# Kernel optimization log

Hardware: AMD Instinct MI355X
Metric: run time of the kernel (lower is better)

## Reference

```python
import jax, jax.numpy as jnp
import numpy as np

N, C, H, W, J = 16, 8, 512, 1024, 8


def setup_inputs() -> dict:
    key = jax.random.key(0)
    logits = jax.random.normal(key, (N, C, H, W), dtype=jnp.float32)
    rng = np.random.default_rng(0)
    start = rng.integers(0, H - 2, size=(N, J))
    length = rng.integers(1, H // 2, size=(N, J))
    end = np.minimum(start + length, H - 1)          # ensure z+1 <= H-1
    ch = rng.integers(0, C, size=(N, J))
    params = jnp.asarray(np.stack([start, end, ch], axis=-1).astype(np.int32))
    return {"logits": logits, "params": params}


def reference(logits, params):
    n, c, h, w = logits.shape
    probs = jax.nn.softmax(logits, axis=-1)
    # soft-argmax expected position over grid axis -> [n, c, h]
    pos = jnp.sum(probs * jnp.arange(w, dtype=logits.dtype), axis=-1)
    # adjacent-row position differences -> [n, c, h-1]
    diff = pos[:, :, :-1] - pos[:, :, 1:]
    start = params[..., 0]   # [n, J]
    end = params[..., 1]     # [n, J]
    ch = params[..., 2]      # [n, J]
    # gather the channel for each (sample, lane): [n, J, h-1]
    diff_g = jnp.take_along_axis(diff, ch[:, :, None].astype(jnp.int32), axis=1)
    z = jnp.arange(h - 1, dtype=jnp.int32)
    mask = (z[None, None, :] >= start[:, :, None]) & (z[None, None, :] < end[:, :, None])
    # smooth_l1 vs zeros, mean over the ragged selected elements
    x = jnp.abs(diff_g)
    sl1 = jnp.where(x < 1.0, 0.5 * diff_g * diff_g, x - 0.5)
    mask_f = mask.astype(logits.dtype)
    total = jnp.sum(sl1 * mask_f)
    count = jnp.sum(mask_f)
    return total / count
```

## Files before the change

kernel.cpp:

```cpp
#include <hip/hip_runtime.h>

#define PN 16
#define PC 8
#define PH 512
#define PW 1024
#define PJ 8

#define NROWS (PN * PC * PH)
#define NPAIRS (PN * PJ)

__global__ __launch_bounds__(256) void pos_kernel(const float* __restrict__ logits,
                                                  const int* __restrict__ params,
                                                  float* __restrict__ pos) {
    const int p = blockIdx.x >> 4;
    const int g = blockIdx.x & 15;

    const int start = params[p * 3 + 0];
    const int end   = params[p * 3 + 1];
    const int ch    = params[p * 3 + 2];

    const int h0 = start + (g << 4);
    if (h0 > end) return;

    const int n = p >> 3;
    const int base_row = (n * PC + ch) * PH;

    const int wave = threadIdx.x >> 6;
    const int lane = threadIdx.x & 63;
    const int grp = lane >> 4;
    const int sub = lane & 15;

    int h = h0 + (wave << 2) + grp;
    if (h > end) h = end;
    const int row_id = base_row + h;
    const float* row = logits + (size_t)row_id * PW;

    float4 v[16];
#pragma unroll
    for (int q = 0; q < 16; ++q)
        v[q] = *reinterpret_cast<const float4*>(row + q * 64 + sub * 4);

    float s = 0.f, sw = 0.f;
#pragma unroll
    for (int q = 0; q < 16; ++q) {
        const float base = (float)(q * 64 + sub * 4);
        float e0 = __expf(v[q].x);
        float e1 = __expf(v[q].y);
        float e2 = __expf(v[q].z);
        float e3 = __expf(v[q].w);
        s += e0 + e1 + e2 + e3;
        sw += e0 * base + e1 * (base + 1.f) + e2 * (base + 2.f) + e3 * (base + 3.f);
    }
#pragma unroll
    for (int off = 8; off > 0; off >>= 1) {
        s += __shfl_xor(s, off);
        sw += __shfl_xor(sw, off);
    }

    if (sub == 0) pos[row_id] = sw / s;
}

__global__ __launch_bounds__(64) void loss_kernel(const float* __restrict__ pos,
                                                  const int* __restrict__ params,
                                                  float* __restrict__ partial) {
    const int nj = blockIdx.x;
    const int start = params[nj * 3 + 0];
    const int end   = params[nj * 3 + 1];
    const int ch    = params[nj * 3 + 2];

    const float* p = pos + ((size_t)(nj >> 3) * PC + ch) * PH;

    float sum = 0.f, cnt = 0.f;
    for (int z = start + (int)threadIdx.x; z < end; z += 64) {
        float d = p[z] - p[z + 1];
        float x = fabsf(d);
        sum += (x < 1.f) ? 0.5f * d * d : (x - 0.5f);
        cnt += 1.f;
    }
#pragma unroll
    for (int off = 32; off > 0; off >>= 1) {
        sum += __shfl_xor(sum, off);
        cnt += __shfl_xor(cnt, off);
    }
    if (threadIdx.x == 0) {
        partial[nj * 2 + 0] = sum;
        partial[nj * 2 + 1] = cnt;
    }
}

__global__ __launch_bounds__(64) void finalize_kernel(const float* __restrict__ partial,
                                                      float* __restrict__ out) {
    const int t = threadIdx.x;
    float s = partial[t * 2 + 0] + partial[(t + 64) * 2 + 0];
    float c = partial[t * 2 + 1] + partial[(t + 64) * 2 + 1];
#pragma unroll
    for (int off = 32; off > 0; off >>= 1) {
        s += __shfl_xor(s, off);
        c += __shfl_xor(c, off);
    }
    if (t == 0) out[0] = s / c;
}

extern "C" void kernel_launch(void* const* d_in, const int* in_sizes, int n_in,
                              void* d_out, int out_size, void* d_ws, size_t ws_size,
                              hipStream_t stream) {
    const float* logits = (const float*)d_in[0];
    const int* params = (const int*)d_in[1];
    float* out = (float*)d_out;

    float* pos = (float*)d_ws;
    float* partial = pos + NROWS;

    pos_kernel<<<NPAIRS * 16, 256, 0, stream>>>(logits, params, pos);
    loss_kernel<<<NPAIRS, 64, 0, stream>>>(pos, params, partial);
    finalize_kernel<<<1, 64, 0, stream>>>(partial, out);
}
```

Measured before the change: 22.26 us.

## Fuse soft-argmax position and smooth-L1 loss into one kernel with overlapping chunks

Merges the position kernel and the loss kernel so each block computes 16 row positions into shared memory and directly emits the smooth-L1 partial sum over its 15 adjacent differences. Chunks overlap by one row to cover boundary differences, and the finalize kernel is widened to reduce the larger number of partials. This removes one kernel launch and the global round trip of the position buffer, at the cost of re-reading one overlap row per chunk and a wider final reduction.

```diff
diff --git a/kernel.cpp b/kernel.cpp
--- a/kernel.cpp
+++ b/kernel.cpp
@@ -6,21 +6,28 @@
 #define PW 1024
 #define PJ 8
 
-#define NROWS (PN * PC * PH)
 #define NPAIRS (PN * PJ)
+#define CHUNKS 17
+#define NPART (NPAIRS * CHUNKS)
 
-__global__ __launch_bounds__(256) void pos_kernel(const float* __restrict__ logits,
-                                                  const int* __restrict__ params,
-                                                  float* __restrict__ pos) {
-    const int p = blockIdx.x >> 4;
-    const int g = blockIdx.x & 15;
+__global__ __launch_bounds__(256) void posloss_kernel(const float* __restrict__ logits,
+                                                      const int* __restrict__ params,
+                                                      float* __restrict__ partial) {
+    const int p = blockIdx.x / CHUNKS;
+    const int g = blockIdx.x % CHUNKS;
 
     const int start = params[p * 3 + 0];
     const int end   = params[p * 3 + 1];
     const int ch    = params[p * 3 + 2];
 
-    const int h0 = start + (g << 4);
-    if (h0 > end) return;
+    const int h0 = start + g * 15;
+    if (h0 > end - 1) {
+        if (threadIdx.x == 0) {
+            partial[blockIdx.x * 2 + 0] = 0.f;
+            partial[blockIdx.x * 2 + 1] = 0.f;
+        }
+        return;
+    }
 
     const int n = p >> 3;
     const int base_row = (n * PC + ch) * PH;
@@ -29,11 +36,11 @@
     const int lane = threadIdx.x & 63;
     const int grp = lane >> 4;
     const int sub = lane & 15;
+    const int r = (wave << 2) | grp;
 
-    int h = h0 + (wave << 2) + grp;
+    int h = h0 + r;
     if (h > end) h = end;
-    const int row_id = base_row + h;
-    const float* row = logits + (size_t)row_id * PW;
+    const float* row = logits + (size_t)(base_row + h) * PW;
 
     float4 v[16];
 #pragma unroll
@@ -57,48 +64,57 @@
         sw += __shfl_xor(sw, off);
     }
 
-    if (sub == 0) pos[row_id] = sw / s;
-}
+    __shared__ float ppos[16];
+    if (sub == 0) ppos[r] = sw / s;
+    __syncthreads();
 
-__global__ __launch_bounds__(64) void loss_kernel(const float* __restrict__ pos,
-                                                  const int* __restrict__ params,
-                                                  float* __restrict__ partial) {
-    const int nj = blockIdx.x;
-    const int start = params[nj * 3 + 0];
-    const int end   = params[nj * 3 + 1];
-    const int ch    = params[nj * 3 + 2];
-
-    const float* p = pos + ((size_t)(nj >> 3) * PC + ch) * PH;
-
-    float sum = 0.f, cnt = 0.f;
-    for (int z = start + (int)threadIdx.x; z < end; z += 64) {
-        float d = p[z] - p[z + 1];
-        float x = fabsf(d);
-        sum += (x < 1.f) ? 0.5f * d * d : (x - 0.5f);
-        cnt += 1.f;
-    }
+    if (threadIdx.x < 64) {
+        int zmax_r = end - 1 - h0;
+        if (zmax_r > 14) zmax_r = 14;
+        float sum = 0.f, cnt = 0.f;
+        if (lane <= zmax_r) {
+            const float d = ppos[lane] - ppos[lane + 1];
+            const float x = fabsf(d);
+            sum = (x < 1.f) ? 0.5f * d * d : (x - 0.5f);
+            cnt = 1.f;
+        }
 #pragma unroll
-    for (int off = 32; off > 0; off >>= 1) {
-        sum += __shfl_xor(sum, off);
-        cnt += __shfl_xor(cnt, off);
-    }
-    if (threadIdx.x == 0) {
-        partial[nj * 2 + 0] = sum;
-        partial[nj * 2 + 1] = cnt;
+        for (int off = 8; off > 0; off >>= 1) {
+            sum += __shfl_xor(sum, off);
+            cnt += __shfl_xor(cnt, off);
+        }
+        if (lane == 0) {
+            partial[blockIdx.x * 2 + 0] = sum;
+            partial[blockIdx.x * 2 + 1] = cnt;
+        }
     }
 }
 
-__global__ __launch_bounds__(64) void finalize_kernel(const float* __restrict__ partial,
-                                                      float* __restrict__ out) {
+__global__ __launch_bounds__(1024) void finalize_kernel(const float* __restrict__ partial,
+                                                        float* __restrict__ out) {
+    __shared__ float ss[16], sc[16];
     const int t = threadIdx.x;
-    float s = partial[t * 2 + 0] + partial[(t + 64) * 2 + 0];
-    float c = partial[t * 2 + 1] + partial[(t + 64) * 2 + 1];
+    const int wave = t >> 6;
+    const int lane = t & 63;
+
+    float s = 0.f, c = 0.f;
+    for (int i = t; i < NPART; i += 1024) {
+        s += partial[2 * i + 0];
+        c += partial[2 * i + 1];
+    }
 #pragma unroll
     for (int off = 32; off > 0; off >>= 1) {
         s += __shfl_xor(s, off);
         c += __shfl_xor(c, off);
     }
-    if (t == 0) out[0] = s / c;
+    if (lane == 0) { ss[wave] = s; sc[wave] = c; }
+    __syncthreads();
+    if (t == 0) {
+        float S = 0.f, C = 0.f;
+#pragma unroll
+        for (int i = 0; i < 16; ++i) { S += ss[i]; C += sc[i]; }
+        out[0] = S / C;
+    }
 }
 
 extern "C" void kernel_launch(void* const* d_in, const int* in_sizes, int n_in,
@@ -108,10 +124,8 @@
     const int* params = (const int*)d_in[1];
     float* out = (float*)d_out;
 
-    float* pos = (float*)d_ws;
-    float* partial = pos + NROWS;
+    float* partial = (float*)d_ws;
 
-    pos_kernel<<<NPAIRS * 16, 256, 0, stream>>>(logits, params, pos);
-    loss_kernel<<<NPAIRS, 64, 0, stream>>>(pos, params, partial);
-    finalize_kernel<<<1, 64, 0, stream>>>(partial, out);
+    posloss_kernel<<<NPART, 256, 0, stream>>>(logits, params, partial);
+    finalize_kernel<<<1, 1024, 0, stream>>>(partial, out);
 }
```

After: 18.67 us, median of 2. 16.1% less time.
